# Optimization experiments

Measured on AMD Instinct MI355X. Metric: run time of the kernel, lower is better.

The kernel has to match this reference:

```python
import jax, jax.numpy as jnp
import numpy as np

B, S, D = 8, 4096, 512
BLOCK, LEFT, RIGHT = 64, 1, 1
FF = 2048
EPS = 1e-6


def setup_inputs() -> dict:
    key = jax.random.key(0)
    ks = jax.random.split(key, 16)
    sd = 1.0 / np.sqrt(D)
    sf = 1.0 / np.sqrt(FF)
    return {
        "x": jax.random.normal(ks[0], (B, S, D), jnp.float32),
        "Wq": jax.random.normal(ks[1], (D, D), jnp.float32) * sd,
        "bq": jnp.zeros((D,), jnp.float32),
        "Wk": jax.random.normal(ks[2], (D, D), jnp.float32) * sd,
        "bk": jnp.zeros((D,), jnp.float32),
        "Wv": jax.random.normal(ks[3], (D, D), jnp.float32) * sd,
        "bv": jnp.zeros((D,), jnp.float32),
        "W1": jax.random.normal(ks[4], (D, FF), jnp.float32) * sd,
        "b1": jnp.zeros((FF,), jnp.float32),
        "W2": jax.random.normal(ks[5], (FF, D), jnp.float32) * sf,
        "b2": jnp.zeros((D,), jnp.float32),
        "g1": jnp.ones((D,), jnp.float32),
        "be1": jnp.zeros((D,), jnp.float32),
        "g2": jnp.ones((D,), jnp.float32),
        "be2": jnp.zeros((D,), jnp.float32),
    }


def layernorm(x, g, b):
    m = jnp.mean(x, axis=-1, keepdims=True)
    v = jnp.mean(jnp.square(x - m), axis=-1, keepdims=True)
    return g * (x - m) * jax.lax.rsqrt(v + EPS) + b


def local_attention(x, Wq, bq, Wk, bk, Wv, bv):
    Bsz, Sl, Dm = x.shape
    nb = Sl // BLOCK          # number of blocks
    nw = LEFT + RIGHT + 1     # window (in blocks)
    q = (x @ Wq + bq).reshape(Bsz, nb, BLOCK, Dm)
    k = (x @ Wk + bk).reshape(Bsz, nb, BLOCK, Dm)
    v = (x @ Wv + bv).reshape(Bsz, nb, BLOCK, Dm)
    # pad block axis so every query block has LEFT/RIGHT neighbor blocks
    kp = jnp.pad(k, ((0, 0), (LEFT, RIGHT), (0, 0), (0, 0)))
    vp = jnp.pad(v, ((0, 0), (LEFT, RIGHT), (0, 0), (0, 0)))
    # gather windows: (B, nb, nw*BLOCK, D)
    k_win = jnp.stack([kp[:, j:j + nb] for j in range(nw)], axis=2).reshape(Bsz, nb, nw * BLOCK, Dm)
    v_win = jnp.stack([vp[:, j:j + nb] for j in range(nw)], axis=2).reshape(Bsz, nb, nw * BLOCK, Dm)
    # mask out-of-range (padded) blocks at sequence edges
    blk = jnp.arange(nb)[:, None] + jnp.arange(nw)[None, :] - LEFT  # (nb, nw)
    mask = ((blk >= 0) & (blk < nb))
    mask = jnp.repeat(mask, BLOCK, axis=1)  # (nb, nw*BLOCK)
    scores = jnp.einsum('bnqd,bnkd->bnqk', q, k_win) / jnp.sqrt(jnp.float32(Dm))
    scores = jnp.where(mask[None, :, None, :], scores, jnp.float32(-1e9))
    attn = jax.nn.softmax(scores, axis=-1)
    out = jnp.einsum('bnqk,bnkd->bnqd', attn, v_win)
    return out.reshape(Bsz, Sl, Dm)


def reference(x, Wq, bq, Wk, bk, Wv, bv, W1, b1, W2, b2, g1, be1, g2, be2):
    # inference mode: dropout is identity
    a = local_attention(x, Wq, bq, Wk, bk, Wv, bv)
    out1 = layernorm(x + a, g1, be1)
    ffn = jnp.maximum(out1 @ W1 + b1, 0.0) @ W2 + b2
    return layernorm(out1 + ffn, g2, be2)
```

## Files before the change

kernel.cpp:

```cpp
#include <hip/hip_runtime.h>


typedef __bf16 bf16;
typedef __bf16 bf16x8 __attribute__((ext_vector_type(8)));
typedef float  f32x4  __attribute__((ext_vector_type(4)));

#define DEV __device__ __forceinline__

#define BAR()  do { asm volatile("" ::: "memory"); __builtin_amdgcn_s_barrier(); asm volatile("" ::: "memory"); } while (0)
#define WAITV0() asm volatile("s_waitcnt vmcnt(0)" ::: "memory")

DEV void gload_lds16(const void* g, void* lds) {
  __builtin_amdgcn_global_load_lds(
      (const __attribute__((address_space(1))) void*)g,
      (__attribute__((address_space(3))) void*)lds, 16, 0, 0);
}

__global__ __launch_bounds__(256) void cast_to_bf16(const float* __restrict__ in,
                                                    bf16* __restrict__ out, int n8) {
  int i = blockIdx.x * 256 + threadIdx.x;
  if (i >= n8) return;
  float4 a0 = ((const float4*)in)[i * 2];
  float4 a1 = ((const float4*)in)[i * 2 + 1];
  bf16x8 o;
  o[0] = (bf16)a0.x; o[1] = (bf16)a0.y; o[2] = (bf16)a0.z; o[3] = (bf16)a0.w;
  o[4] = (bf16)a1.x; o[5] = (bf16)a1.y; o[6] = (bf16)a1.z; o[7] = (bf16)a1.w;
  ((bf16x8*)out)[i] = o;
}

__global__ __launch_bounds__(256) void transpose_cast(const float* __restrict__ W,
                                                      bf16* __restrict__ Wt, int K, int N) {
  __shared__ bf16 tile[64][66];
  const int n0 = blockIdx.x * 64, k0 = blockIdx.y * 64;
  const int t = threadIdx.x;
#pragma unroll
  for (int it = 0; it < 16; ++it) {
    int c = it * 256 + t;
    int kr = c >> 6, nc = c & 63;
    tile[nc][kr] = (bf16)W[(size_t)(k0 + kr) * N + n0 + nc];
  }
  __syncthreads();
#pragma unroll
  for (int it = 0; it < 2; ++it) {
    int c = it * 256 + t;
    int nr = c >> 3, kg = (c & 7) * 8;
    bf16x8 v;
#pragma unroll
    for (int e = 0; e < 8; ++e) v[e] = tile[nr][kg + e];
    *(bf16x8*)(Wt + (size_t)(n0 + nr) * K + k0 + kg) = v;
  }
}

__global__ __launch_bounds__(256) void concat_bias(const float* __restrict__ bq,
                                                   const float* __restrict__ bk,
                                                   const float* __restrict__ bv,
                                                   float* __restrict__ o) {
  int i = blockIdx.x * 256 + threadIdx.x;
  if (i < 512) o[i] = bq[i];
  else if (i < 1024) o[i] = bk[i - 512];
  else if (i < 1536) o[i] = bv[i - 1024];
}

template <int RELU, int F32OUT>
__global__ __launch_bounds__(512, 2)
void gemm256(const bf16* __restrict__ A, const bf16* __restrict__ Bt,
             const float* __restrict__ bias, void* __restrict__ Cout,
             int M, int N, int K) {
  __shared__ bf16x8 lds8[8192];
  char* const LB = (char*)lds8;
  const int tid = threadIdx.x;
  const int w = tid >> 6, l = tid & 63;
  const int lr = l & 15, lg = l >> 4;
  const int wm = w >> 2, wn = w & 3;

  const int bid = blockIdx.y * gridDim.x + blockIdx.x;
  const int NX = gridDim.y;
  const int xcd = bid & 7;
  const int idx = bid >> 3;
  const int mi = idx / NX;
  const int nn = idx - mi * NX;
  const int m0 = (xcd * 16 + mi) * 256;
  const int n0 = nn * 256;

  const int NT = K >> 6;

  int srow[4], scol[4];
#pragma unroll
  for (int j = 0; j < 4; ++j) {
    const int sg = tid + 512 * j;
    srow[j] = sg >> 3;
    scol[j] = (((sg & 7) ^ ((sg >> 3) & 7)) << 3);
  }

  const int swz0 = ((lg ^ (lr & 7)) << 4);
  const int swz1 = (((4 | lg) ^ (lr & 7)) << 4);

  f32x4 acc[8][4];
#pragma unroll
  for (int i = 0; i < 8; ++i)
#pragma unroll
    for (int j = 0; j < 4; ++j) acc[i][j] = f32x4{0.f, 0.f, 0.f, 0.f};

  auto stage = [&](int t) {
    char* dA = LB + ((t & 1) << 16) + tid * 16;
#pragma unroll
    for (int j = 0; j < 4; ++j) {
      gload_lds16(A + (size_t)(m0 + srow[j]) * K + t * 64 + scol[j], dA + j * 8192);
      gload_lds16(Bt + (size_t)(n0 + srow[j]) * K + t * 64 + scol[j], dA + 32768 + j * 8192);
    }
  };

  stage(0);
  WAITV0();
  BAR();

  for (int t = 0; t < NT; ++t) {
    if (t + 1 < NT) stage(t + 1);
    const char* base = LB + ((t & 1) << 16);
    const char* pA = base + (wm << 14) + (lr << 7);
    const char* pB = base + 32768 + (wn << 13) + (lr << 7);
    bf16x8 bv_[4][2];
#pragma unroll
    for (int n = 0; n < 4; ++n) {
      bv_[n][0] = *(const bf16x8*)(pB + n * 2048 + swz0);
      bv_[n][1] = *(const bf16x8*)(pB + n * 2048 + swz1);
    }
#pragma unroll
    for (int i = 0; i < 8; ++i) {
      bf16x8 a0 = *(const bf16x8*)(pA + i * 2048 + swz0);
      bf16x8 a1 = *(const bf16x8*)(pA + i * 2048 + swz1);
#pragma unroll
      for (int n = 0; n < 4; ++n) {
        acc[i][n] = __builtin_amdgcn_mfma_f32_16x16x32_bf16(a0, bv_[n][0], acc[i][n], 0, 0, 0);
        acc[i][n] = __builtin_amdgcn_mfma_f32_16x16x32_bf16(a1, bv_[n][1], acc[i][n], 0, 0, 0);
      }
    }
    WAITV0();
    BAR();
  }

  if (!F32OUT) {
    bf16* cl = (bf16*)LB;
    bf16* Cb = (bf16*)Cout;
#pragma unroll
    for (int half = 0; half < 2; ++half) {
      if (wm == half) {
#pragma unroll
        for (int n = 0; n < 4; ++n) {
          const int col = (wn << 6) + (n << 4) + lr;
          const float bv = bias[n0 + col];
#pragma unroll
          for (int m = 0; m < 8; ++m)
#pragma unroll
            for (int rg = 0; rg < 4; ++rg) {
              const int row = (m << 4) + (lg << 2) + rg;
              float v = acc[m][n][rg] + bv;
              if (RELU) v = fmaxf(v, 0.f);
              cl[row * 264 + col] = (bf16)v;
            }
        }
      }
      __syncthreads();
#pragma unroll
      for (int it = 0; it < 8; ++it) {
        const int idx2 = it * 512 + tid;
        const int r = idx2 >> 5, ch = idx2 & 31;
        *(bf16x8*)(Cb + (size_t)(m0 + half * 128 + r) * N + n0 + (ch << 3)) =
            *(const bf16x8*)(cl + r * 264 + (ch << 3));
      }
      __syncthreads();
    }
  } else {
    float* Cf = (float*)Cout;
#pragma unroll
    for (int n = 0; n < 4; ++n) {
      const int col = n0 + (wn << 6) + (n << 4) + lr;
      const float bv = bias[col];
#pragma unroll
      for (int m = 0; m < 8; ++m)
#pragma unroll
        for (int rg = 0; rg < 4; ++rg) {
          const int row = m0 + (wm << 7) + (m << 4) + (lg << 2) + rg;
          float v = acc[m][n][rg] + bv;
          if (RELU) v = fmaxf(v, 0.f);
          Cf[(size_t)row * N + col] = v;
        }
    }
  }
}

__global__ __launch_bounds__(256) void transpose_v(const bf16* __restrict__ qkv,
                                                   bf16* __restrict__ vt) {
  __shared__ bf16 tile[64][66];
  const int s0 = blockIdx.x * 64, d0 = blockIdx.y * 64, b = blockIdx.z;
  const int t = threadIdx.x;
#pragma unroll
  for (int it = 0; it < 2; ++it) {
    int c = it * 256 + t;
    int r = c >> 3, g = (c & 7) * 8;
    bf16x8 v = *(const bf16x8*)(qkv + ((size_t)b * 4096 + s0 + r) * 1536 + 1024 + d0 + g);
#pragma unroll
    for (int e = 0; e < 8; ++e) tile[g + e][r] = v[e];
  }
  __syncthreads();
#pragma unroll
  for (int it = 0; it < 2; ++it) {
    int c = it * 256 + t;
    int dr = c >> 3, sg = (c & 7) * 8;
    bf16x8 v;
#pragma unroll
    for (int e = 0; e < 8; ++e) v[e] = tile[dr][sg + e];
    *(bf16x8*)(vt + ((size_t)b * 512 + d0 + dr) * 4096 + s0 + sg) = v;
  }
}

__global__ __launch_bounds__(512, 4)
void attn_local(const bf16* __restrict__ qkv, const bf16* __restrict__ vt,
                bf16* __restrict__ aout) {
  __shared__ bf16 P[4][16][200];
  __shared__ float xmx[4][2][16];
  __shared__ float xsm[4][2][16];
  const int qb = blockIdx.x, b = blockIdx.y;
  const int t = threadIdx.x, w = t >> 6, l = t & 63;
  const int rg = w & 3, h = w >> 2;
  const int lr = l & 15, lg = l >> 4;

  bool val[6];
#pragma unroll
  for (int n = 0; n < 6; ++n) {
    int gn = 6 * h + n;
    val[n] = ((unsigned)(qb - 1 + (gn >> 2)) < 64u);
  }

  const size_t qrow = (size_t)b * 4096 + qb * 64 + rg * 16;
  const bf16* qp = qkv + (qrow + lr) * 1536 + lg * 8;
  const bf16* kbase = qkv + ((long)b * 4096 + (long)(qb - 1) * 64) * 1536 + 512;

  f32x4 S[6];
#pragma unroll
  for (int n = 0; n < 6; ++n) S[n] = f32x4{0.f, 0.f, 0.f, 0.f};

  for (int kk = 0; kk < 16; ++kk) {
    bf16x8 aq = *(const bf16x8*)(qp + kk * 32);
#pragma unroll
    for (int n = 0; n < 6; ++n) {
      if (!val[n]) continue;
      const int gn = 6 * h + n;
      bf16x8 bk = *(const bf16x8*)(kbase + (size_t)(gn * 16 + lr) * 1536 + kk * 32 + lg * 8);
      S[n] = __builtin_amdgcn_mfma_f32_16x16x32_bf16(aq, bk, S[n], 0, 0, 0);
    }
  }

  const float scale = 0.044194173824159216f;
  float mx[4] = {-3e38f, -3e38f, -3e38f, -3e38f};
#pragma unroll
  for (int n = 0; n < 6; ++n) {
    if (!val[n]) continue;
#pragma unroll
    for (int i = 0; i < 4; ++i) mx[i] = fmaxf(mx[i], S[n][i]);
  }
#pragma unroll
  for (int i = 0; i < 4; ++i) {
    mx[i] = fmaxf(mx[i], __shfl_xor(mx[i], 1));
    mx[i] = fmaxf(mx[i], __shfl_xor(mx[i], 2));
    mx[i] = fmaxf(mx[i], __shfl_xor(mx[i], 4));
    mx[i] = fmaxf(mx[i], __shfl_xor(mx[i], 8));
  }
  if (lr == 0) {
#pragma unroll
    for (int i = 0; i < 4; ++i) xmx[rg][h][lg * 4 + i] = mx[i];
  }
  __syncthreads();
  float m4[4];
#pragma unroll
  for (int i = 0; i < 4; ++i) m4[i] = fmaxf(mx[i], xmx[rg][h ^ 1][lg * 4 + i]);

  float sm[4] = {0.f, 0.f, 0.f, 0.f};
#pragma unroll
  for (int n = 0; n < 6; ++n) {
    if (!val[n]) continue;
#pragma unroll
    for (int i = 0; i < 4; ++i) {
      float p = __expf((S[n][i] - m4[i]) * scale);
      S[n][i] = p;
      sm[i] += p;
    }
  }
#pragma unroll
  for (int i = 0; i < 4; ++i) {
    sm[i] += __shfl_xor(sm[i], 1);
    sm[i] += __shfl_xor(sm[i], 2);
    sm[i] += __shfl_xor(sm[i], 4);
    sm[i] += __shfl_xor(sm[i], 8);
  }
  if (lr == 0) {
#pragma unroll
    for (int i = 0; i < 4; ++i) xsm[rg][h][lg * 4 + i] = sm[i];
  }
  __syncthreads();
  float rinv[4];
#pragma unroll
  for (int i = 0; i < 4; ++i) rinv[i] = 1.f / (sm[i] + xsm[rg][h ^ 1][lg * 4 + i]);

#pragma unroll
  for (int n = 0; n < 6; ++n) {
    const int gn = 6 * h + n;
#pragma unroll
    for (int i = 0; i < 4; ++i)
      P[rg][lg * 4 + i][gn * 16 + lr] = val[n] ? (bf16)(S[n][i] * rinv[i]) : (bf16)0.f;
  }
  __syncthreads();

  f32x4 O[4][4];
#pragma unroll
  for (int rt = 0; rt < 4; ++rt)
#pragma unroll
    for (int dt = 0; dt < 4; ++dt) O[rt][dt] = f32x4{0.f, 0.f, 0.f, 0.f};

  const bf16* vtb = vt + ((long)b * 512 + w * 64) * 4096 + (long)(qb - 1) * 64;
#pragma unroll
  for (int ks = 0; ks < 6; ++ks) {
    if ((unsigned)(qb - 1 + (ks >> 1)) >= 64u) continue;
    bf16x8 vf[4];
#pragma unroll
    for (int dt = 0; dt < 4; ++dt)
      vf[dt] = *(const bf16x8*)(vtb + (size_t)(dt * 16 + lr) * 4096 + ks * 32 + lg * 8);
#pragma unroll
    for (int rt = 0; rt < 4; ++rt) {
      bf16x8 pa = *(const bf16x8*)&P[rt][lr][ks * 32 + lg * 8];
#pragma unroll
      for (int dt = 0; dt < 4; ++dt)
        O[rt][dt] = __builtin_amdgcn_mfma_f32_16x16x32_bf16(pa, vf[dt], O[rt][dt], 0, 0, 0);
    }
  }

  const size_t orow = (size_t)b * 4096 + qb * 64;
#pragma unroll
  for (int rt = 0; rt < 4; ++rt)
#pragma unroll
    for (int dt = 0; dt < 4; ++dt)
#pragma unroll
      for (int i = 0; i < 4; ++i)
        aout[(orow + rt * 16 + lg * 4 + i) * 512 + w * 64 + dt * 16 + lr] =
            (bf16)O[rt][dt][i];
}

__global__ __launch_bounds__(256) void ln_res1(const float* __restrict__ x,
                                               const bf16* __restrict__ a,
                                               const float* __restrict__ g,
                                               const float* __restrict__ be,
                                               bf16* __restrict__ out) {
  const int t = threadIdx.x, w = t >> 6, l = t & 63;
  const size_t row = (size_t)blockIdx.x * 4 + w;
  const float* xp = x + row * 512 + l * 8;
  float4 x0 = ((const float4*)xp)[0];
  float4 x1 = ((const float4*)xp)[1];
  bf16x8 av = *(const bf16x8*)(a + row * 512 + l * 8);
  float s[8] = {x0.x + (float)av[0], x0.y + (float)av[1], x0.z + (float)av[2], x0.w + (float)av[3],
                x1.x + (float)av[4], x1.y + (float)av[5], x1.z + (float)av[6], x1.w + (float)av[7]};
  float sum = 0.f;
#pragma unroll
  for (int i = 0; i < 8; ++i) sum += s[i];
#pragma unroll
  for (int m = 1; m <= 32; m <<= 1) sum += __shfl_xor(sum, m);
  const float mean = sum * (1.f / 512.f);
  float vs = 0.f;
#pragma unroll
  for (int i = 0; i < 8; ++i) { float d = s[i] - mean; vs += d * d; }
#pragma unroll
  for (int m = 1; m <= 32; m <<= 1) vs += __shfl_xor(vs, m);
  const float r = rsqrtf(vs * (1.f / 512.f) + 1e-6f);
  float4 g0 = ((const float4*)(g + l * 8))[0], g1 = ((const float4*)(g + l * 8))[1];
  float4 b0 = ((const float4*)(be + l * 8))[0], b1 = ((const float4*)(be + l * 8))[1];
  bf16x8 o;
  o[0] = (bf16)(g0.x * (s[0] - mean) * r + b0.x);
  o[1] = (bf16)(g0.y * (s[1] - mean) * r + b0.y);
  o[2] = (bf16)(g0.z * (s[2] - mean) * r + b0.z);
  o[3] = (bf16)(g0.w * (s[3] - mean) * r + b0.w);
  o[4] = (bf16)(g1.x * (s[4] - mean) * r + b1.x);
  o[5] = (bf16)(g1.y * (s[5] - mean) * r + b1.y);
  o[6] = (bf16)(g1.z * (s[6] - mean) * r + b1.z);
  o[7] = (bf16)(g1.w * (s[7] - mean) * r + b1.w);
  *(bf16x8*)(out + row * 512 + l * 8) = o;
}

__global__ __launch_bounds__(256) void ln_res2(const bf16* __restrict__ o1,
                                               float* __restrict__ y,
                                               const float* __restrict__ g,
                                               const float* __restrict__ be) {
  const int t = threadIdx.x, w = t >> 6, l = t & 63;
  const size_t row = (size_t)blockIdx.x * 4 + w;
  float* yp = y + row * 512 + l * 8;
  float4 y0 = ((const float4*)yp)[0];
  float4 y1 = ((const float4*)yp)[1];
  bf16x8 ov = *(const bf16x8*)(o1 + row * 512 + l * 8);
  float s[8] = {y0.x + (float)ov[0], y0.y + (float)ov[1], y0.z + (float)ov[2], y0.w + (float)ov[3],
                y1.x + (float)ov[4], y1.y + (float)ov[5], y1.z + (float)ov[6], y1.w + (float)ov[7]};
  float sum = 0.f;
#pragma unroll
  for (int i = 0; i < 8; ++i) sum += s[i];
#pragma unroll
  for (int m = 1; m <= 32; m <<= 1) sum += __shfl_xor(sum, m);
  const float mean = sum * (1.f / 512.f);
  float vs = 0.f;
#pragma unroll
  for (int i = 0; i < 8; ++i) { float d = s[i] - mean; vs += d * d; }
#pragma unroll
  for (int m = 1; m <= 32; m <<= 1) vs += __shfl_xor(vs, m);
  const float r = rsqrtf(vs * (1.f / 512.f) + 1e-6f);
  float4 g0 = ((const float4*)(g + l * 8))[0], g1 = ((const float4*)(g + l * 8))[1];
  float4 b0 = ((const float4*)(be + l * 8))[0], b1 = ((const float4*)(be + l * 8))[1];
  float4 r0, r1;
  r0.x = g0.x * (s[0] - mean) * r + b0.x;
  r0.y = g0.y * (s[1] - mean) * r + b0.y;
  r0.z = g0.z * (s[2] - mean) * r + b0.z;
  r0.w = g0.w * (s[3] - mean) * r + b0.w;
  r1.x = g1.x * (s[4] - mean) * r + b1.x;
  r1.y = g1.y * (s[5] - mean) * r + b1.y;
  r1.z = g1.z * (s[6] - mean) * r + b1.z;
  r1.w = g1.w * (s[7] - mean) * r + b1.w;
  ((float4*)yp)[0] = r0;
  ((float4*)yp)[1] = r1;
}

extern "C" void kernel_launch(void* const* d_in, const int* in_sizes, int n_in,
                              void* d_out, int out_size, void* d_ws, size_t ws_size,
                              hipStream_t stream) {
  const float* x   = (const float*)d_in[0];
  const float* Wq  = (const float*)d_in[1];
  const float* bq  = (const float*)d_in[2];
  const float* Wk  = (const float*)d_in[3];
  const float* bk  = (const float*)d_in[4];
  const float* Wv  = (const float*)d_in[5];
  const float* bv  = (const float*)d_in[6];
  const float* W1  = (const float*)d_in[7];
  const float* b1  = (const float*)d_in[8];
  const float* W2  = (const float*)d_in[9];
  const float* b2  = (const float*)d_in[10];
  const float* g1  = (const float*)d_in[11];
  const float* be1 = (const float*)d_in[12];
  const float* g2  = (const float*)d_in[13];
  const float* be2 = (const float*)d_in[14];
  float* out = (float*)d_out;

  char* ws = (char*)d_ws;
  bf16*  WqkvT = (bf16*)(ws + 0);
  bf16*  W1T   = (bf16*)(ws + 1572864);
  bf16*  W2T   = (bf16*)(ws + 3670016);
  float* bqkv  = (float*)(ws + 5767168);
  bf16*  xb    = (bf16*)(ws + 6291456);
  bf16*  out1  = (bf16*)(ws + 39845888);
  bf16*  qkv   = (bf16*)(ws + 73400320);
  bf16*  vtb   = (bf16*)(ws + 174063616);
  bf16*  a_    = xb;
  bf16*  h     = qkv;

  cast_to_bf16<<<8192, 256, 0, stream>>>(x, xb, 2097152);
  transpose_cast<<<dim3(8, 8), 256, 0, stream>>>(Wq, WqkvT, 512, 512);
  transpose_cast<<<dim3(8, 8), 256, 0, stream>>>(Wk, WqkvT + 262144, 512, 512);
  transpose_cast<<<dim3(8, 8), 256, 0, stream>>>(Wv, WqkvT + 524288, 512, 512);
  transpose_cast<<<dim3(32, 8), 256, 0, stream>>>(W1, W1T, 512, 2048);
  transpose_cast<<<dim3(8, 32), 256, 0, stream>>>(W2, W2T, 2048, 512);
  concat_bias<<<6, 256, 0, stream>>>(bq, bk, bv, bqkv);

  gemm256<0, 0><<<dim3(128, 6), 512, 0, stream>>>(xb, WqkvT, bqkv, qkv, 32768, 1536, 512);
  transpose_v<<<dim3(64, 8, 8), 256, 0, stream>>>(qkv, vtb);
  attn_local<<<dim3(64, 8), 512, 0, stream>>>(qkv, vtb, a_);
  ln_res1<<<8192, 256, 0, stream>>>(x, a_, g1, be1, out1);
  gemm256<1, 0><<<dim3(128, 8), 512, 0, stream>>>(out1, W1T, b1, h, 32768, 2048, 512);
  gemm256<0, 1><<<dim3(128, 2), 512, 0, stream>>>(h, W2T, b2, out, 32768, 512, 2048);
  ln_res2<<<8192, 256, 0, stream>>>(out1, out, g2, be2);
}
```

Before: 401.7 us.

## Shrink GEMM tiles to 128x128 and load B operand directly from global

Replaces the 256x256, 512-thread GEMM with a 128x128, 256-thread version at higher occupancy. Only A is staged into LDS through double buffering. Each wave now reads its B fragments straight from global memory into registers, which cuts LDS use and brings more blocks onto the GPU. In exchange, B reuse through LDS is lost, so B traffic goes through the caches, and per-block arithmetic intensity drops.

```diff
diff --git a/kernel.cpp b/kernel.cpp
--- a/kernel.cpp
+++ b/kernel.cpp
@@ -62,16 +62,15 @@
 }
 
 template <int RELU, int F32OUT>
-__global__ __launch_bounds__(512, 2)
-void gemm256(const bf16* __restrict__ A, const bf16* __restrict__ Bt,
+__global__ __launch_bounds__(256, 3)
+void gemm128(const bf16* __restrict__ A, const bf16* __restrict__ Bt,
              const float* __restrict__ bias, void* __restrict__ Cout,
              int M, int N, int K) {
-  __shared__ bf16x8 lds8[8192];
-  char* const LB = (char*)lds8;
+  __shared__ char LB[32768];
   const int tid = threadIdx.x;
   const int w = tid >> 6, l = tid & 63;
   const int lr = l & 15, lg = l >> 4;
-  const int wm = w >> 2, wn = w & 3;
+  const int wm = w >> 1, wn = w & 1;
 
   const int bid = blockIdx.y * gridDim.x + blockIdx.x;
   const int NX = gridDim.y;
@@ -79,54 +78,53 @@
   const int idx = bid >> 3;
   const int mi = idx / NX;
   const int nn = idx - mi * NX;
-  const int m0 = (xcd * 16 + mi) * 256;
-  const int n0 = nn * 256;
+  const int m0 = (xcd * 32 + mi) * 128;
+  const int n0 = nn * 128;
 
   const int NT = K >> 6;
 
   int srow[4], scol[4];
 #pragma unroll
   for (int j = 0; j < 4; ++j) {
-    const int sg = tid + 512 * j;
-    srow[j] = sg >> 3;
-    scol[j] = (((sg & 7) ^ ((sg >> 3) & 7)) << 3);
+    const int s = tid + 256 * j;
+    srow[j] = s >> 3;
+    scol[j] = (((s & 7) ^ ((s >> 3) & 7)) << 3);
   }
 
   const int swz0 = ((lg ^ (lr & 7)) << 4);
   const int swz1 = (((4 | lg) ^ (lr & 7)) << 4);
 
-  f32x4 acc[8][4];
-#pragma unroll
-  for (int i = 0; i < 8; ++i)
+  f32x4 acc[4][4];
+#pragma unroll
+  for (int i = 0; i < 4; ++i)
 #pragma unroll
     for (int j = 0; j < 4; ++j) acc[i][j] = f32x4{0.f, 0.f, 0.f, 0.f};
 
   auto stage = [&](int t) {
-    char* dA = LB + ((t & 1) << 16) + tid * 16;
-#pragma unroll
-    for (int j = 0; j < 4; ++j) {
-      gload_lds16(A + (size_t)(m0 + srow[j]) * K + t * 64 + scol[j], dA + j * 8192);
-      gload_lds16(Bt + (size_t)(n0 + srow[j]) * K + t * 64 + scol[j], dA + 32768 + j * 8192);
-    }
+    char* d = LB + ((t & 1) << 14) + tid * 16;
+#pragma unroll
+    for (int j = 0; j < 4; ++j)
+      gload_lds16(A + (size_t)(m0 + srow[j]) * K + t * 64 + scol[j], d + j * 4096);
   };
+
+  const bf16* Bw = Bt + (size_t)(n0 + wn * 64 + lr) * K;
 
   stage(0);
   WAITV0();
   BAR();
 
   for (int t = 0; t < NT; ++t) {
+    bf16x8 bv_[4][2];
+#pragma unroll
+    for (int n = 0; n < 4; ++n) {
+      const bf16* bp = Bw + (size_t)(n * 16) * K + t * 64 + lg * 8;
+      bv_[n][0] = *(const bf16x8*)(bp);
+      bv_[n][1] = *(const bf16x8*)(bp + 32);
+    }
     if (t + 1 < NT) stage(t + 1);
-    const char* base = LB + ((t & 1) << 16);
-    const char* pA = base + (wm << 14) + (lr << 7);
-    const char* pB = base + 32768 + (wn << 13) + (lr << 7);
-    bf16x8 bv_[4][2];
-#pragma unroll
-    for (int n = 0; n < 4; ++n) {
-      bv_[n][0] = *(const bf16x8*)(pB + n * 2048 + swz0);
-      bv_[n][1] = *(const bf16x8*)(pB + n * 2048 + swz1);
-    }
-#pragma unroll
-    for (int i = 0; i < 8; ++i) {
+    const char* pA = LB + ((t & 1) << 14) + (((wm << 6) + lr) << 7);
+#pragma unroll
+    for (int i = 0; i < 4; ++i) {
       bf16x8 a0 = *(const bf16x8*)(pA + i * 2048 + swz0);
       bf16x8 a1 = *(const bf16x8*)(pA + i * 2048 + swz1);
 #pragma unroll
@@ -150,23 +148,23 @@
           const int col = (wn << 6) + (n << 4) + lr;
           const float bv = bias[n0 + col];
 #pragma unroll
-          for (int m = 0; m < 8; ++m)
+          for (int i = 0; i < 4; ++i)
 #pragma unroll
             for (int rg = 0; rg < 4; ++rg) {
-              const int row = (m << 4) + (lg << 2) + rg;
-              float v = acc[m][n][rg] + bv;
+              const int row = (i << 4) + (lg << 2) + rg;
+              float v = acc[i][n][rg] + bv;
               if (RELU) v = fmaxf(v, 0.f);
-              cl[row * 264 + col] = (bf16)v;
+              cl[row * 136 + col] = (bf16)v;
             }
         }
       }
       __syncthreads();
 #pragma unroll
-      for (int it = 0; it < 8; ++it) {
-        const int idx2 = it * 512 + tid;
-        const int r = idx2 >> 5, ch = idx2 & 31;
-        *(bf16x8*)(Cb + (size_t)(m0 + half * 128 + r) * N + n0 + (ch << 3)) =
-            *(const bf16x8*)(cl + r * 264 + (ch << 3));
+      for (int it = 0; it < 4; ++it) {
+        const int idx2 = it * 256 + tid;
+        const int r = idx2 >> 4, c = idx2 & 15;
+        *(bf16x8*)(Cb + (size_t)(m0 + half * 64 + r) * N + n0 + (c << 3)) =
+            *(const bf16x8*)(cl + r * 136 + (c << 3));
       }
       __syncthreads();
     }
@@ -177,11 +175,11 @@
       const int col = n0 + (wn << 6) + (n << 4) + lr;
       const float bv = bias[col];
 #pragma unroll
-      for (int m = 0; m < 8; ++m)
+      for (int i = 0; i < 4; ++i)
 #pragma unroll
         for (int rg = 0; rg < 4; ++rg) {
-          const int row = m0 + (wm << 7) + (m << 4) + (lg << 2) + rg;
-          float v = acc[m][n][rg] + bv;
+          const int row = m0 + (wm << 6) + (i << 4) + (lg << 2) + rg;
+          float v = acc[i][n][rg] + bv;
           if (RELU) v = fmaxf(v, 0.f);
           Cf[(size_t)row * N + col] = v;
         }
@@ -463,11 +461,11 @@
   transpose_cast<<<dim3(8, 32), 256, 0, stream>>>(W2, W2T, 2048, 512);
   concat_bias<<<6, 256, 0, stream>>>(bq, bk, bv, bqkv);
 
-  gemm256<0, 0><<<dim3(128, 6), 512, 0, stream>>>(xb, WqkvT, bqkv, qkv, 32768, 1536, 512);
+  gemm128<0, 0><<<dim3(256, 12), 256, 0, stream>>>(xb, WqkvT, bqkv, qkv, 32768, 1536, 512);
   transpose_v<<<dim3(64, 8, 8), 256, 0, stream>>>(qkv, vtb);
   attn_local<<<dim3(64, 8), 512, 0, stream>>>(qkv, vtb, a_);
   ln_res1<<<8192, 256, 0, stream>>>(x, a_, g1, be1, out1);
-  gemm256<1, 0><<<dim3(128, 8), 512, 0, stream>>>(out1, W1T, b1, h, 32768, 2048, 512);
-  gemm256<0, 1><<<dim3(128, 2), 512, 0, stream>>>(h, W2T, b2, out, 32768, 512, 2048);
+  gemm128<1, 0><<<dim3(256, 16), 256, 0, stream>>>(out1, W1T, b1, h, 32768, 2048, 512);
+  gemm128<0, 1><<<dim3(256, 4), 256, 0, stream>>>(h, W2T, b2, out, 32768, 512, 2048);
   ln_res2<<<8192, 256, 0, stream>>>(out1, out, g2, be2);
 }
```

Measured after the change: 568.2 us. 41.5% more time.

## Triple-buffer A tiles in GEMM with two-deep prefetch and partial vmcnt waits

Applied to the files above, without the earlier changes.

The GEMM kernel now splits staging into A and B loaders. It triple-buffers the A tile in a 160KB LDS allocation so A can be prefetched two K-steps ahead, while B stays double-buffered. The end-of-iteration wait now allows the newest A loads to stay in flight, which hides more global load latency. In exchange, the larger LDS footprint drops occupancy from two blocks per CU to one, so there is less inter-block latency hiding.

```diff
diff --git a/kernel.cpp b/kernel.cpp
--- a/kernel.cpp
+++ b/kernel.cpp
@@ -8,6 +8,7 @@
 #define DEV __device__ __forceinline__
 
 #define BAR()  do { asm volatile("" ::: "memory"); __builtin_amdgcn_s_barrier(); asm volatile("" ::: "memory"); } while (0)
+#define WAITV(n) asm volatile("s_waitcnt vmcnt(" #n ")" ::: "memory")
 #define WAITV0() asm volatile("s_waitcnt vmcnt(0)" ::: "memory")
 
 DEV void gload_lds16(const void* g, void* lds) {
@@ -62,12 +63,11 @@
 }
 
 template <int RELU, int F32OUT>
-__global__ __launch_bounds__(512, 2)
+__global__ __launch_bounds__(512, 1)
 void gemm256(const bf16* __restrict__ A, const bf16* __restrict__ Bt,
              const float* __restrict__ bias, void* __restrict__ Cout,
              int M, int N, int K) {
-  __shared__ bf16x8 lds8[8192];
-  char* const LB = (char*)lds8;
+  __shared__ char LB[163840];
   const int tid = threadIdx.x;
   const int w = tid >> 6, l = tid & 63;
   const int lr = l & 15, lg = l >> 4;
@@ -87,9 +87,9 @@
   int srow[4], scol[4];
 #pragma unroll
   for (int j = 0; j < 4; ++j) {
-    const int sg = tid + 512 * j;
-    srow[j] = sg >> 3;
-    scol[j] = (((sg & 7) ^ ((sg >> 3) & 7)) << 3);
+    const int s = tid + 512 * j;
+    srow[j] = s >> 3;
+    scol[j] = (((s & 7) ^ ((s >> 3) & 7)) << 3);
   }
 
   const int swz0 = ((lg ^ (lr & 7)) << 4);
@@ -101,24 +101,28 @@
 #pragma unroll
     for (int j = 0; j < 4; ++j) acc[i][j] = f32x4{0.f, 0.f, 0.f, 0.f};
 
-  auto stage = [&](int t) {
-    char* dA = LB + ((t & 1) << 16) + tid * 16;
-#pragma unroll
-    for (int j = 0; j < 4; ++j) {
-      gload_lds16(A + (size_t)(m0 + srow[j]) * K + t * 64 + scol[j], dA + j * 8192);
-      gload_lds16(Bt + (size_t)(n0 + srow[j]) * K + t * 64 + scol[j], dA + 32768 + j * 8192);
-    }
+  auto stageA = [&](int t) {
+    char* d = LB + (t % 3) * 32768 + tid * 16;
+#pragma unroll
+    for (int j = 0; j < 4; ++j)
+      gload_lds16(A + (size_t)(m0 + srow[j]) * K + t * 64 + scol[j], d + j * 8192);
   };
-
-  stage(0);
-  WAITV0();
+  auto stageB = [&](int t) {
+    char* d = LB + 98304 + (t & 1) * 32768 + tid * 16;
+#pragma unroll
+    for (int j = 0; j < 4; ++j)
+      gload_lds16(Bt + (size_t)(n0 + srow[j]) * K + t * 64 + scol[j], d + j * 8192);
+  };
+
+  stageA(0); stageB(0); stageA(1);
+  WAITV(4);
   BAR();
 
   for (int t = 0; t < NT; ++t) {
-    if (t + 1 < NT) stage(t + 1);
-    const char* base = LB + ((t & 1) << 16);
-    const char* pA = base + (wm << 14) + (lr << 7);
-    const char* pB = base + 32768 + (wn << 13) + (lr << 7);
+    if (t + 1 < NT) stageB(t + 1);
+    if (t + 2 < NT) stageA(t + 2);
+    const char* pA = LB + (t % 3) * 32768 + (wm << 14) + (lr << 7);
+    const char* pB = LB + 98304 + (t & 1) * 32768 + (wn << 13) + (lr << 7);
     bf16x8 bv_[4][2];
 #pragma unroll
     for (int n = 0; n < 4; ++n) {
@@ -135,7 +139,8 @@
         acc[i][n] = __builtin_amdgcn_mfma_f32_16x16x32_bf16(a1, bv_[n][1], acc[i][n], 0, 0, 0);
       }
     }
-    WAITV0();
+    if (t + 2 < NT) { WAITV(4); }
+    else { WAITV0(); }
     BAR();
   }
 
```

After: 397.0 us. No clear change (-1.2%).

## Halve GEMM K-tile to 32 and raise occupancy to 4 blocks per CU

Applied to the files above, without the earlier changes.

The 256x256 bf16 GEMM now stages K-tiles of 32 instead of 64, which halves the per-buffer LDS footprint from 64KB to 32KB. It uses a new swizzle in which two rows share a 128-byte line. The launch bound goes from 2 to 4 waves-per-EU so more blocks can be resident and hide global-load latency. The cost is twice as many barrier and wait iterations, less MFMA work per sync, and tighter register limits that may cause spills. The LDS array is sized at 69632 bytes, which also leaves room for the epilogue.

```diff
diff --git a/kernel.cpp b/kernel.cpp
--- a/kernel.cpp
+++ b/kernel.cpp
@@ -62,12 +62,11 @@
 }
 
 template <int RELU, int F32OUT>
-__global__ __launch_bounds__(512, 2)
+__global__ __launch_bounds__(512, 4)
 void gemm256(const bf16* __restrict__ A, const bf16* __restrict__ Bt,
              const float* __restrict__ bias, void* __restrict__ Cout,
              int M, int N, int K) {
-  __shared__ bf16x8 lds8[8192];
-  char* const LB = (char*)lds8;
+  __shared__ char LB[69632];
   const int tid = threadIdx.x;
   const int w = tid >> 6, l = tid & 63;
   const int lr = l & 15, lg = l >> 4;
@@ -82,18 +81,18 @@
   const int m0 = (xcd * 16 + mi) * 256;
   const int n0 = nn * 256;
 
-  const int NT = K >> 6;
-
-  int srow[4], scol[4];
-#pragma unroll
-  for (int j = 0; j < 4; ++j) {
-    const int sg = tid + 512 * j;
-    srow[j] = sg >> 3;
-    scol[j] = (((sg & 7) ^ ((sg >> 3) & 7)) << 3);
-  }
-
-  const int swz0 = ((lg ^ (lr & 7)) << 4);
-  const int swz1 = (((4 | lg) ^ (lr & 7)) << 4);
+  const int NT = K >> 5;
+
+  int srow[2], scol[2];
+#pragma unroll
+  for (int j = 0; j < 2; ++j) {
+    const int s = tid + 512 * j;
+    const int jr = s >> 3, u = (s & 7) ^ (jr & 7);
+    srow[j] = 2 * jr + (u >> 2);
+    scol[j] = (u & 3) << 3;
+  }
+
+  const int off = ((lr >> 1) << 7) + (((lg + ((lr & 1) << 2)) ^ (lr >> 1)) << 4);
 
   f32x4 acc[8][4];
 #pragma unroll
@@ -102,11 +101,11 @@
     for (int j = 0; j < 4; ++j) acc[i][j] = f32x4{0.f, 0.f, 0.f, 0.f};
 
   auto stage = [&](int t) {
-    char* dA = LB + ((t & 1) << 16) + tid * 16;
-#pragma unroll
-    for (int j = 0; j < 4; ++j) {
-      gload_lds16(A + (size_t)(m0 + srow[j]) * K + t * 64 + scol[j], dA + j * 8192);
-      gload_lds16(Bt + (size_t)(n0 + srow[j]) * K + t * 64 + scol[j], dA + 32768 + j * 8192);
+    char* d = LB + ((t & 1) << 15) + tid * 16;
+#pragma unroll
+    for (int j = 0; j < 2; ++j) {
+      gload_lds16(A + (size_t)(m0 + srow[j]) * K + t * 32 + scol[j], d + j * 8192);
+      gload_lds16(Bt + (size_t)(n0 + srow[j]) * K + t * 32 + scol[j], d + 16384 + j * 8192);
     }
   };
 
@@ -116,24 +115,19 @@
 
   for (int t = 0; t < NT; ++t) {
     if (t + 1 < NT) stage(t + 1);
-    const char* base = LB + ((t & 1) << 16);
-    const char* pA = base + (wm << 14) + (lr << 7);
-    const char* pB = base + 32768 + (wn << 13) + (lr << 7);
-    bf16x8 bv_[4][2];
-#pragma unroll
-    for (int n = 0; n < 4; ++n) {
-      bv_[n][0] = *(const bf16x8*)(pB + n * 2048 + swz0);
-      bv_[n][1] = *(const bf16x8*)(pB + n * 2048 + swz1);
-    }
+    const char* base = LB + ((t & 1) << 15);
+    const char* pA = base + (wm << 13) + off;
+    const char* pB = base + 16384 + (wn << 12) + off;
+    bf16x8 bv_[4];
+#pragma unroll
+    for (int n = 0; n < 4; ++n)
+      bv_[n] = *(const bf16x8*)(pB + n * 1024);
 #pragma unroll
     for (int i = 0; i < 8; ++i) {
-      bf16x8 a0 = *(const bf16x8*)(pA + i * 2048 + swz0);
-      bf16x8 a1 = *(const bf16x8*)(pA + i * 2048 + swz1);
-#pragma unroll
-      for (int n = 0; n < 4; ++n) {
-        acc[i][n] = __builtin_amdgcn_mfma_f32_16x16x32_bf16(a0, bv_[n][0], acc[i][n], 0, 0, 0);
-        acc[i][n] = __builtin_amdgcn_mfma_f32_16x16x32_bf16(a1, bv_[n][1], acc[i][n], 0, 0, 0);
-      }
+      bf16x8 a0 = *(const bf16x8*)(pA + i * 1024);
+#pragma unroll
+      for (int n = 0; n < 4; ++n)
+        acc[i][n] = __builtin_amdgcn_mfma_f32_16x16x32_bf16(a0, bv_[n], acc[i][n], 0, 0, 0);
     }
     WAITV0();
     BAR();
```

Result: slower. 1.299 ms (+223.4%).
